# Kernel optimization log

Hardware: AMD Instinct MI355X
Metric: run time of the kernel (lower is better)

Reference implementation:

```python
import jax, jax.numpy as jnp
import numpy as np

NUM_NODES = 50000
NUM_REL_ORIG = 5            # original relation types
NUM_REL = 2 * NUM_REL_ORIG + 1  # augmented: original + inverse + self-loop = 11
F_IN = 128
F_OUT = 128
NUM_EDGES = 800000


def setup_inputs() -> dict:
    key = jax.random.key(0)
    k1, k2, k3, k4, k5, k6 = jax.random.split(key, 6)
    src = jax.random.randint(k1, (NUM_EDGES,), 0, NUM_NODES, dtype=jnp.int32)
    rel = jax.random.randint(k2, (NUM_EDGES,), 0, NUM_REL_ORIG, dtype=jnp.int32)
    dst = jax.random.randint(k3, (NUM_EDGES,), 0, NUM_NODES, dtype=jnp.int32)
    graph = jnp.stack([src, rel, dst], axis=1)  # [E, 3] = (head, relation, tail)
    features = jax.random.normal(k4, (NUM_NODES, F_IN), dtype=jnp.float32)
    # RGCNConv parameters (no basis/block decomposition, bias=False, root_weight=True)
    glorot = lambda k, shape: jax.random.normal(k, shape, dtype=jnp.float32) * jnp.sqrt(2.0 / (shape[-2] + shape[-1]))
    weight = glorot(k5, (NUM_REL, F_IN, F_OUT))  # per-relation weights
    root = glorot(k6, (F_IN, F_OUT))             # root (self) weight
    return {"graph": graph, "features": features, "weight": weight, "root": root}


def reference(graph, features, weight, root):
    N = features.shape[0]
    R = weight.shape[0]
    n_orig = (R - 1) // 2
    src, rel, dst = graph[:, 0], graph[:, 1], graph[:, 2]
    loop = jnp.arange(N, dtype=graph.dtype)
    # augmented edge list: original, inverse, self-loops
    full_src = jnp.concatenate([src, dst, loop])
    full_dst = jnp.concatenate([dst, src, loop])
    full_rel = jnp.concatenate([rel, rel + n_orig, jnp.full((N,), 2 * n_orig, dtype=graph.dtype)])
    # per-(relation, dst-node) mean of source features (PyG RGCNConv aggr='mean'
    # aggregates raw x_j per relation, then applies W_r to the aggregate)
    seg = full_rel * N + full_dst  # [E_full]
    msgs = features[full_src]      # [E_full, F_in] gather
    sums = jax.ops.segment_sum(msgs, seg, num_segments=R * N)           # [R*N, F_in]
    cnts = jax.ops.segment_sum(jnp.ones((seg.shape[0],), features.dtype), seg, num_segments=R * N)
    mean = sums / jnp.maximum(cnts, 1.0)[:, None]
    mean = mean.reshape(R, N, -1)  # [R, N, F_in]
    # out = sum_r mean_r @ W_r + x @ W_root
    out = jnp.einsum('rnf,rfo->no', mean, weight) + features @ root
    return out
```

## Files before the change

### kernel.cpp

```cpp
#include <hip/hip_runtime.h>
#include <hip/hip_bf16.h>

#define NN 50000
#define RO 5
#define RT 11
#define FF 128
#define EE 800000
#define EE2 (2 * EE)
#define NBINS (2 * RO * NN)
#define SLOTS 32
#define DPB 32
#define FEAT_BLKS ((NN * FF / 4) / 256)
#define WT_BLKS ((RT * FF * FF) / 256)

typedef unsigned short u16;
typedef unsigned int u32;
typedef __attribute__((ext_vector_type(4))) unsigned short u16x4;
typedef __attribute__((ext_vector_type(4))) unsigned int u32x4;
typedef __attribute__((ext_vector_type(8))) short bf16x8;
typedef __attribute__((ext_vector_type(4))) float f32x4;

__device__ __forceinline__ u16 f2b(float x) {
  unsigned u = __float_as_uint(x);
  return (u16)((u + 0x7fffu + ((u >> 16) & 1u)) >> 16);
}

__global__ __launch_bounds__(256) void prep_k(const float* __restrict__ f,
                                              const float* __restrict__ w,
                                              const float* __restrict__ root,
                                              u16* __restrict__ fb,
                                              u16* __restrict__ wt) {
  int b = blockIdx.x;
  if (b < FEAT_BLKS) {
    int i = b * 256 + threadIdx.x;
    float4 v = reinterpret_cast<const float4*>(f)[i];
    u16x4 o;
    o.x = f2b(v.x); o.y = f2b(v.y); o.z = f2b(v.z); o.w = f2b(v.w);
    reinterpret_cast<u16x4*>(fb)[i] = o;
  } else if (b < FEAT_BLKS + WT_BLKS) {
    int idx = (b - FEAT_BLKS) * 256 + threadIdx.x;
    int r = idx >> 14;
    int rem = idx & 16383;
    int k = rem >> 7;
    int o = rem & 127;
    float v = w[idx];
    if (r == 10) v += root[rem];
    int chunk = (k >> 3) ^ (o & 7);
    wt[(r << 14) + (o << 7) + (chunk << 3) + (k & 7)] = f2b(v);
  } else {
    if (threadIdx.x < 64) reinterpret_cast<u32*>(fb)[NN * 64 + threadIdx.x] = 0;
  }
}

__global__ __launch_bounds__(256) void fill_k(const int* __restrict__ g,
                                              int* __restrict__ cur,
                                              u16* __restrict__ eidx) {
  const int m = blockIdx.x * 256 + threadIdx.x;
  int e, bin; u16 val;
  if (m < EE) {
    e = m;
    int s = g[3 * e], r = g[3 * e + 1], d = g[3 * e + 2];
    bin = r * NN + d; val = (u16)s;
  } else {
    e = m - EE;
    int d2 = g[3 * e], r = g[3 * e + 1], s2 = g[3 * e + 2];
    bin = (r + RO) * NN + d2; val = (u16)s2;
  }
  int pos = atomicAdd(&cur[bin], 1);
  if (pos < SLOTS) eidx[bin * SLOTS + pos] = val;
}

#define ACCX(p) { a0 += __uint_as_float((p).x << 16); a1 += __uint_as_float((p).x & 0xffff0000u); \
                  a2 += __uint_as_float((p).y << 16); a3 += __uint_as_float((p).y & 0xffff0000u); \
                  a4 += __uint_as_float((p).z << 16); a5 += __uint_as_float((p).z & 0xffff0000u); \
                  a6 += __uint_as_float((p).w << 16); a7 += __uint_as_float((p).w & 0xffff0000u); }
#define ACCY(p) { b0 += __uint_as_float((p).x << 16); b1 += __uint_as_float((p).x & 0xffff0000u); \
                  b2 += __uint_as_float((p).y << 16); b3 += __uint_as_float((p).y & 0xffff0000u); \
                  b4 += __uint_as_float((p).z << 16); b5 += __uint_as_float((p).z & 0xffff0000u); \
                  b6 += __uint_as_float((p).w << 16); b7 += __uint_as_float((p).w & 0xffff0000u); }

__global__ __launch_bounds__(256) void mg_k(const int* __restrict__ cnt,
                                            const u32* __restrict__ eidx32,
                                            const u32x4* __restrict__ fv4,
                                            const u16* __restrict__ fbf,
                                            const u16* __restrict__ wt,
                                            float* __restrict__ out) {
  __shared__ __align__(16) u32x4 Asw[DPB * 16];
  const int tid  = threadIdx.x;
  const int lane = tid & 63;
  const int wv   = tid >> 6;
  const int l15  = lane & 15;
  const int ko   = lane >> 4;
  const int qid  = wv * 4 + ko;
  const int q16  = ko << 4;
  const int base = blockIdx.x * DPB;

  f32x4 acc[2][2];
#pragma unroll
  for (int i = 0; i < 2; ++i)
#pragma unroll
    for (int j = 0; j < 2; ++j) acc[i][j] = (f32x4){0.f, 0.f, 0.f, 0.f};

  const int row0 = qid * 2, row1 = row0 + 1;
  const int d0 = base + row0, d1 = base + row1;
  const bool v0 = d0 < NN, v1 = d1 < NN;

  for (int r = 0; r < 10; ++r) {
    const int seg0 = v0 ? r * NN + d0 : 0;
    const int seg1 = v1 ? r * NN + d1 : 0;
    const int c0 = v0 ? min(cnt[seg0], SLOTS) : 0;
    const int c1 = v1 ? min(cnt[seg1], SLOTS) : 0;
    const u32 sl0 = eidx32[seg0 * 16 + l15];
    const u32 sl1 = eidx32[seg1 * 16 + l15];
    int cmax = max(c0, c1);
    cmax = max(cmax, __shfl_xor(cmax, 16));
    cmax = max(cmax, __shfl_xor(cmax, 32));

    float a0 = 0.f, a1 = 0.f, a2 = 0.f, a3 = 0.f, a4 = 0.f, a5 = 0.f, a6 = 0.f, a7 = 0.f;
    float b0 = 0.f, b1 = 0.f, b2 = 0.f, b3 = 0.f, b4 = 0.f, b5 = 0.f, b6 = 0.f, b7 = 0.f;

    for (int i = 0; i < cmax; i += 4) {
      u32 wa0 = __shfl(sl0, q16 + (i >> 1));
      u32 wa1 = __shfl(sl0, q16 + (i >> 1) + 1);
      u32 wb0 = __shfl(sl1, q16 + (i >> 1));
      u32 wb1 = __shfl(sl1, q16 + (i >> 1) + 1);
      int s0 = (i     < c0) ? (int)(wa0 & 0xffffu) : NN;
      int s1 = (i + 1 < c0) ? (int)(wa0 >> 16)     : NN;
      int s2 = (i + 2 < c0) ? (int)(wa1 & 0xffffu) : NN;
      int s3 = (i + 3 < c0) ? (int)(wa1 >> 16)     : NN;
      int t0 = (i     < c1) ? (int)(wb0 & 0xffffu) : NN;
      int t1 = (i + 1 < c1) ? (int)(wb0 >> 16)     : NN;
      int t2 = (i + 2 < c1) ? (int)(wb1 & 0xffffu) : NN;
      int t3 = (i + 3 < c1) ? (int)(wb1 >> 16)     : NN;
      u32x4 p0 = fv4[s0 * 16 + l15];
      u32x4 p1 = fv4[s1 * 16 + l15];
      u32x4 p2 = fv4[s2 * 16 + l15];
      u32x4 p3 = fv4[s3 * 16 + l15];
      u32x4 p4 = fv4[t0 * 16 + l15];
      u32x4 p5 = fv4[t1 * 16 + l15];
      u32x4 p6 = fv4[t2 * 16 + l15];
      u32x4 p7 = fv4[t3 * 16 + l15];
      ACCX(p0); ACCX(p1); ACCX(p2); ACCX(p3);
      ACCY(p4); ACCY(p5); ACCY(p6); ACCY(p7);
    }

    const float i0 = (c0 > 0) ? 1.0f / (float)c0 : 0.0f;
    const float i1 = (c1 > 0) ? 1.0f / (float)c1 : 0.0f;
    u32x4 m0, m1;
    m0.x = (u32)f2b(a0 * i0) | ((u32)f2b(a1 * i0) << 16);
    m0.y = (u32)f2b(a2 * i0) | ((u32)f2b(a3 * i0) << 16);
    m0.z = (u32)f2b(a4 * i0) | ((u32)f2b(a5 * i0) << 16);
    m0.w = (u32)f2b(a6 * i0) | ((u32)f2b(a7 * i0) << 16);
    m1.x = (u32)f2b(b0 * i1) | ((u32)f2b(b1 * i1) << 16);
    m1.y = (u32)f2b(b2 * i1) | ((u32)f2b(b3 * i1) << 16);
    m1.z = (u32)f2b(b4 * i1) | ((u32)f2b(b5 * i1) << 16);
    m1.w = (u32)f2b(b6 * i1) | ((u32)f2b(b7 * i1) << 16);
    Asw[row0 * 16 + (l15 ^ (row0 & 7))] = m0;
    Asw[row1 * 16 + (l15 ^ (row1 & 7))] = m1;
    __syncthreads();

    const u16* wb = wt + (r << 14);
#pragma unroll
    for (int kc = 0; kc < 4; ++kc) {
      bf16x8 afr[2];
#pragma unroll
      for (int fq = 0; fq < 2; ++fq) {
        const int arow = fq * 16 + l15;
        afr[fq] = *reinterpret_cast<const bf16x8*>(
            &Asw[arow * 16 + ((kc * 4 + ko) ^ (arow & 7))]);
      }
#pragma unroll
      for (int fr = 0; fr < 2; ++fr) {
        const int o = wv * 32 + fr * 16 + l15;
        bf16x8 b = *reinterpret_cast<const bf16x8*>(
            wb + (o << 7) + (((kc * 4 + ko) ^ (o & 7)) << 3));
        acc[0][fr] = __builtin_amdgcn_mfma_f32_16x16x32_bf16(afr[0], b, acc[0][fr], 0, 0, 0);
        acc[1][fr] = __builtin_amdgcn_mfma_f32_16x16x32_bf16(afr[1], b, acc[1][fr], 0, 0, 0);
      }
    }
    __syncthreads();
  }

  {
    const u16* wb = wt + (10 << 14);
#pragma unroll
    for (int kc = 0; kc < 4; ++kc) {
      bf16x8 afr[2];
#pragma unroll
      for (int fq = 0; fq < 2; ++fq) {
        int rowg = base + fq * 16 + l15;
        rowg = (rowg < NN) ? rowg : NN;
        afr[fq] = *reinterpret_cast<const bf16x8*>(
            fbf + (long)rowg * FF + kc * 32 + ko * 8);
      }
#pragma unroll
      for (int fr = 0; fr < 2; ++fr) {
        const int o = wv * 32 + fr * 16 + l15;
        bf16x8 b = *reinterpret_cast<const bf16x8*>(
            wb + (o << 7) + (((kc * 4 + ko) ^ (o & 7)) << 3));
        acc[0][fr] = __builtin_amdgcn_mfma_f32_16x16x32_bf16(afr[0], b, acc[0][fr], 0, 0, 0);
        acc[1][fr] = __builtin_amdgcn_mfma_f32_16x16x32_bf16(afr[1], b, acc[1][fr], 0, 0, 0);
      }
    }
  }

#pragma unroll
  for (int fq = 0; fq < 2; ++fq)
#pragma unroll
    for (int fr = 0; fr < 2; ++fr)
#pragma unroll
      for (int q2 = 0; q2 < 4; ++q2) {
        const int row = base + fq * 16 + ko * 4 + q2;
        if (row < NN) out[row * FF + wv * 32 + fr * 16 + l15] = acc[fq][fr][q2];
      }
}

extern "C" void kernel_launch(void* const* d_in, const int* in_sizes, int n_in,
                              void* d_out, int out_size, void* d_ws, size_t ws_size,
                              hipStream_t stream) {
  const int*   graph  = (const int*)d_in[0];
  const float* feat   = (const float*)d_in[1];
  const float* weight = (const float*)d_in[2];
  const float* root   = (const float*)d_in[3];
  float* out = (float*)d_out;
  char* ws = (char*)d_ws;

  u16* fbf  = (u16*)(ws);
  u16* wt   = (u16*)(ws + 12800512);
  int* cur  = (int*)(ws + 13160960);
  u16* eidx = (u16*)(ws + 15161088);

  hipMemsetAsync(cur, 0, NBINS * sizeof(int), stream);
  prep_k<<<FEAT_BLKS + WT_BLKS + 1, 256, 0, stream>>>(feat, weight, root, fbf, wt);
  fill_k<<<EE2 / 256, 256, 0, stream>>>(graph, cur, eidx);
  mg_k<<<(NN + DPB - 1) / DPB, 256, 0, stream>>>(cur, (const u32*)eidx,
                                                 (const u32x4*)fbf, fbf, wt, out);
}
```

Before: 288.1 us.

## Fuse fill and prep kernels; halve destinations per block in gather-matmul

Merges the edge-bucketing kernel and the feature/weight bf16 conversion kernel into one launch so they can run concurrently. The main kernel now handles 16 destination rows per block instead of 32, so each 16-lane quarter gathers one destination row and the MFMA runs on a single 16-row A tile. The result is twice as many blocks and lower register use, at the cost of reading each weight fragment twice as often overall. Bounds checks are dropped because 50000 divides evenly by 16.

```diff
diff --git a/kernel.cpp b/kernel.cpp
--- a/kernel.cpp
+++ b/kernel.cpp
@@ -9,7 +9,8 @@
 #define EE2 (2 * EE)
 #define NBINS (2 * RO * NN)
 #define SLOTS 32
-#define DPB 32
+#define DPB 16
+#define FILL_BLKS (EE2 / 256)
 #define FEAT_BLKS ((NN * FF / 4) / 256)
 #define WT_BLKS ((RT * FF * FF) / 256)
 
@@ -25,20 +26,37 @@
   return (u16)((u + 0x7fffu + ((u >> 16) & 1u)) >> 16);
 }
 
-__global__ __launch_bounds__(256) void prep_k(const float* __restrict__ f,
-                                              const float* __restrict__ w,
-                                              const float* __restrict__ root,
-                                              u16* __restrict__ fb,
-                                              u16* __restrict__ wt) {
-  int b = blockIdx.x;
-  if (b < FEAT_BLKS) {
-    int i = b * 256 + threadIdx.x;
+__global__ __launch_bounds__(256) void pf_k(const int* __restrict__ g,
+                                            const float* __restrict__ f,
+                                            const float* __restrict__ w,
+                                            const float* __restrict__ root,
+                                            int* __restrict__ cur,
+                                            u16* __restrict__ eidx,
+                                            u16* __restrict__ fb,
+                                            u16* __restrict__ wt) {
+  const int b = blockIdx.x;
+  if (b < FILL_BLKS) {
+    const int m = b * 256 + threadIdx.x;
+    int e, bin; u16 val;
+    if (m < EE) {
+      e = m;
+      int s = g[3 * e], r = g[3 * e + 1], d = g[3 * e + 2];
+      bin = r * NN + d; val = (u16)s;
+    } else {
+      e = m - EE;
+      int d2 = g[3 * e], r = g[3 * e + 1], s2 = g[3 * e + 2];
+      bin = (r + RO) * NN + d2; val = (u16)s2;
+    }
+    int pos = atomicAdd(&cur[bin], 1);
+    if (pos < SLOTS) eidx[bin * SLOTS + pos] = val;
+  } else if (b < FILL_BLKS + FEAT_BLKS) {
+    int i = (b - FILL_BLKS) * 256 + threadIdx.x;
     float4 v = reinterpret_cast<const float4*>(f)[i];
     u16x4 o;
     o.x = f2b(v.x); o.y = f2b(v.y); o.z = f2b(v.z); o.w = f2b(v.w);
     reinterpret_cast<u16x4*>(fb)[i] = o;
-  } else if (b < FEAT_BLKS + WT_BLKS) {
-    int idx = (b - FEAT_BLKS) * 256 + threadIdx.x;
+  } else if (b < FILL_BLKS + FEAT_BLKS + WT_BLKS) {
+    int idx = (b - FILL_BLKS - FEAT_BLKS) * 256 + threadIdx.x;
     int r = idx >> 14;
     int rem = idx & 16383;
     int k = rem >> 7;
@@ -52,32 +70,10 @@
   }
 }
 
-__global__ __launch_bounds__(256) void fill_k(const int* __restrict__ g,
-                                              int* __restrict__ cur,
-                                              u16* __restrict__ eidx) {
-  const int m = blockIdx.x * 256 + threadIdx.x;
-  int e, bin; u16 val;
-  if (m < EE) {
-    e = m;
-    int s = g[3 * e], r = g[3 * e + 1], d = g[3 * e + 2];
-    bin = r * NN + d; val = (u16)s;
-  } else {
-    e = m - EE;
-    int d2 = g[3 * e], r = g[3 * e + 1], s2 = g[3 * e + 2];
-    bin = (r + RO) * NN + d2; val = (u16)s2;
-  }
-  int pos = atomicAdd(&cur[bin], 1);
-  if (pos < SLOTS) eidx[bin * SLOTS + pos] = val;
-}
-
 #define ACCX(p) { a0 += __uint_as_float((p).x << 16); a1 += __uint_as_float((p).x & 0xffff0000u); \
                   a2 += __uint_as_float((p).y << 16); a3 += __uint_as_float((p).y & 0xffff0000u); \
                   a4 += __uint_as_float((p).z << 16); a5 += __uint_as_float((p).z & 0xffff0000u); \
                   a6 += __uint_as_float((p).w << 16); a7 += __uint_as_float((p).w & 0xffff0000u); }
-#define ACCY(p) { b0 += __uint_as_float((p).x << 16); b1 += __uint_as_float((p).x & 0xffff0000u); \
-                  b2 += __uint_as_float((p).y << 16); b3 += __uint_as_float((p).y & 0xffff0000u); \
-                  b4 += __uint_as_float((p).z << 16); b5 += __uint_as_float((p).z & 0xffff0000u); \
-                  b6 += __uint_as_float((p).w << 16); b7 += __uint_as_float((p).w & 0xffff0000u); }
 
 __global__ __launch_bounds__(256) void mg_k(const int* __restrict__ cnt,
                                             const u32* __restrict__ eidx32,
@@ -94,88 +90,55 @@
   const int qid  = wv * 4 + ko;
   const int q16  = ko << 4;
   const int base = blockIdx.x * DPB;
+  const int drow = base + qid;
 
-  f32x4 acc[2][2];
-#pragma unroll
-  for (int i = 0; i < 2; ++i)
-#pragma unroll
-    for (int j = 0; j < 2; ++j) acc[i][j] = (f32x4){0.f, 0.f, 0.f, 0.f};
-
-  const int row0 = qid * 2, row1 = row0 + 1;
-  const int d0 = base + row0, d1 = base + row1;
-  const bool v0 = d0 < NN, v1 = d1 < NN;
+  f32x4 acc[2];
+  acc[0] = (f32x4){0.f, 0.f, 0.f, 0.f};
+  acc[1] = (f32x4){0.f, 0.f, 0.f, 0.f};
 
   for (int r = 0; r < 10; ++r) {
-    const int seg0 = v0 ? r * NN + d0 : 0;
-    const int seg1 = v1 ? r * NN + d1 : 0;
-    const int c0 = v0 ? min(cnt[seg0], SLOTS) : 0;
-    const int c1 = v1 ? min(cnt[seg1], SLOTS) : 0;
-    const u32 sl0 = eidx32[seg0 * 16 + l15];
-    const u32 sl1 = eidx32[seg1 * 16 + l15];
-    int cmax = max(c0, c1);
+    const int seg = r * NN + drow;
+    const int c = min(cnt[seg], SLOTS);
+    const u32 sl = eidx32[seg * 16 + l15];
+    int cmax = c;
     cmax = max(cmax, __shfl_xor(cmax, 16));
     cmax = max(cmax, __shfl_xor(cmax, 32));
 
     float a0 = 0.f, a1 = 0.f, a2 = 0.f, a3 = 0.f, a4 = 0.f, a5 = 0.f, a6 = 0.f, a7 = 0.f;
-    float b0 = 0.f, b1 = 0.f, b2 = 0.f, b3 = 0.f, b4 = 0.f, b5 = 0.f, b6 = 0.f, b7 = 0.f;
-
     for (int i = 0; i < cmax; i += 4) {
-      u32 wa0 = __shfl(sl0, q16 + (i >> 1));
-      u32 wa1 = __shfl(sl0, q16 + (i >> 1) + 1);
-      u32 wb0 = __shfl(sl1, q16 + (i >> 1));
-      u32 wb1 = __shfl(sl1, q16 + (i >> 1) + 1);
-      int s0 = (i     < c0) ? (int)(wa0 & 0xffffu) : NN;
-      int s1 = (i + 1 < c0) ? (int)(wa0 >> 16)     : NN;
-      int s2 = (i + 2 < c0) ? (int)(wa1 & 0xffffu) : NN;
-      int s3 = (i + 3 < c0) ? (int)(wa1 >> 16)     : NN;
-      int t0 = (i     < c1) ? (int)(wb0 & 0xffffu) : NN;
-      int t1 = (i + 1 < c1) ? (int)(wb0 >> 16)     : NN;
-      int t2 = (i + 2 < c1) ? (int)(wb1 & 0xffffu) : NN;
-      int t3 = (i + 3 < c1) ? (int)(wb1 >> 16)     : NN;
+      u32 w0 = __shfl(sl, q16 + (i >> 1));
+      u32 w1 = __shfl(sl, q16 + (i >> 1) + 1);
+      int s0 = (i     < c) ? (int)(w0 & 0xffffu) : NN;
+      int s1 = (i + 1 < c) ? (int)(w0 >> 16)     : NN;
+      int s2 = (i + 2 < c) ? (int)(w1 & 0xffffu) : NN;
+      int s3 = (i + 3 < c) ? (int)(w1 >> 16)     : NN;
       u32x4 p0 = fv4[s0 * 16 + l15];
       u32x4 p1 = fv4[s1 * 16 + l15];
       u32x4 p2 = fv4[s2 * 16 + l15];
       u32x4 p3 = fv4[s3 * 16 + l15];
-      u32x4 p4 = fv4[t0 * 16 + l15];
-      u32x4 p5 = fv4[t1 * 16 + l15];
-      u32x4 p6 = fv4[t2 * 16 + l15];
-      u32x4 p7 = fv4[t3 * 16 + l15];
       ACCX(p0); ACCX(p1); ACCX(p2); ACCX(p3);
-      ACCY(p4); ACCY(p5); ACCY(p6); ACCY(p7);
     }
 
-    const float i0 = (c0 > 0) ? 1.0f / (float)c0 : 0.0f;
-    const float i1 = (c1 > 0) ? 1.0f / (float)c1 : 0.0f;
-    u32x4 m0, m1;
-    m0.x = (u32)f2b(a0 * i0) | ((u32)f2b(a1 * i0) << 16);
-    m0.y = (u32)f2b(a2 * i0) | ((u32)f2b(a3 * i0) << 16);
-    m0.z = (u32)f2b(a4 * i0) | ((u32)f2b(a5 * i0) << 16);
-    m0.w = (u32)f2b(a6 * i0) | ((u32)f2b(a7 * i0) << 16);
-    m1.x = (u32)f2b(b0 * i1) | ((u32)f2b(b1 * i1) << 16);
-    m1.y = (u32)f2b(b2 * i1) | ((u32)f2b(b3 * i1) << 16);
-    m1.z = (u32)f2b(b4 * i1) | ((u32)f2b(b5 * i1) << 16);
-    m1.w = (u32)f2b(b6 * i1) | ((u32)f2b(b7 * i1) << 16);
-    Asw[row0 * 16 + (l15 ^ (row0 & 7))] = m0;
-    Asw[row1 * 16 + (l15 ^ (row1 & 7))] = m1;
+    const float inv = (c > 0) ? 1.0f / (float)c : 0.0f;
+    u32x4 m0;
+    m0.x = (u32)f2b(a0 * inv) | ((u32)f2b(a1 * inv) << 16);
+    m0.y = (u32)f2b(a2 * inv) | ((u32)f2b(a3 * inv) << 16);
+    m0.z = (u32)f2b(a4 * inv) | ((u32)f2b(a5 * inv) << 16);
+    m0.w = (u32)f2b(a6 * inv) | ((u32)f2b(a7 * inv) << 16);
+    Asw[qid * 16 + (l15 ^ (qid & 7))] = m0;
     __syncthreads();
 
     const u16* wb = wt + (r << 14);
 #pragma unroll
     for (int kc = 0; kc < 4; ++kc) {
-      bf16x8 afr[2];
-#pragma unroll
-      for (int fq = 0; fq < 2; ++fq) {
-        const int arow = fq * 16 + l15;
-        afr[fq] = *reinterpret_cast<const bf16x8*>(
-            &Asw[arow * 16 + ((kc * 4 + ko) ^ (arow & 7))]);
-      }
+      bf16x8 a = *reinterpret_cast<const bf16x8*>(
+          &Asw[l15 * 16 + ((kc * 4 + ko) ^ (l15 & 7))]);
 #pragma unroll
       for (int fr = 0; fr < 2; ++fr) {
         const int o = wv * 32 + fr * 16 + l15;
-        bf16x8 b = *reinterpret_cast<const bf16x8*>(
+        bf16x8 bfrag = *reinterpret_cast<const bf16x8*>(
             wb + (o << 7) + (((kc * 4 + ko) ^ (o & 7)) << 3));
-        acc[0][fr] = __builtin_amdgcn_mfma_f32_16x16x32_bf16(afr[0], b, acc[0][fr], 0, 0, 0);
-        acc[1][fr] = __builtin_amdgcn_mfma_f32_16x16x32_bf16(afr[1], b, acc[1][fr], 0, 0, 0);
+        acc[fr] = __builtin_amdgcn_mfma_f32_16x16x32_bf16(a, bfrag, acc[fr], 0, 0, 0);
       }
     }
     __syncthreads();
@@ -185,34 +148,23 @@
     const u16* wb = wt + (10 << 14);
 #pragma unroll
     for (int kc = 0; kc < 4; ++kc) {
-      bf16x8 afr[2];
-#pragma unroll
-      for (int fq = 0; fq < 2; ++fq) {
-        int rowg = base + fq * 16 + l15;
-        rowg = (rowg < NN) ? rowg : NN;
-        afr[fq] = *reinterpret_cast<const bf16x8*>(
-            fbf + (long)rowg * FF + kc * 32 + ko * 8);
-      }
+      bf16x8 a = *reinterpret_cast<const bf16x8*>(
+          fbf + (long)(base + l15) * FF + kc * 32 + ko * 8);
 #pragma unroll
       for (int fr = 0; fr < 2; ++fr) {
         const int o = wv * 32 + fr * 16 + l15;
-        bf16x8 b = *reinterpret_cast<const bf16x8*>(
+        bf16x8 bfrag = *reinterpret_cast<const bf16x8*>(
             wb + (o << 7) + (((kc * 4 + ko) ^ (o & 7)) << 3));
-        acc[0][fr] = __builtin_amdgcn_mfma_f32_16x16x32_bf16(afr[0], b, acc[0][fr], 0, 0, 0);
-        acc[1][fr] = __builtin_amdgcn_mfma_f32_16x16x32_bf16(afr[1], b, acc[1][fr], 0, 0, 0);
+        acc[fr] = __builtin_amdgcn_mfma_f32_16x16x32_bf16(a, bfrag, acc[fr], 0, 0, 0);
       }
     }
   }
 
 #pragma unroll
-  for (int fq = 0; fq < 2; ++fq)
+  for (int fr = 0; fr < 2; ++fr)
 #pragma unroll
-    for (int fr = 0; fr < 2; ++fr)
-#pragma unroll
-      for (int q2 = 0; q2 < 4; ++q2) {
-        const int row = base + fq * 16 + ko * 4 + q2;
-        if (row < NN) out[row * FF + wv * 32 + fr * 16 + l15] = acc[fq][fr][q2];
-      }
+    for (int q2 = 0; q2 < 4; ++q2)
+      out[(base + ko * 4 + q2) * FF + wv * 32 + fr * 16 + l15] = acc[fr][q2];
 }
 
 extern "C" void kernel_launch(void* const* d_in, const int* in_sizes, int n_in,
@@ -231,8 +183,8 @@
   u16* eidx = (u16*)(ws + 15161088);
 
   hipMemsetAsync(cur, 0, NBINS * sizeof(int), stream);
-  prep_k<<<FEAT_BLKS + WT_BLKS + 1, 256, 0, stream>>>(feat, weight, root, fbf, wt);
-  fill_k<<<EE2 / 256, 256, 0, stream>>>(graph, cur, eidx);
-  mg_k<<<(NN + DPB - 1) / DPB, 256, 0, stream>>>(cur, (const u32*)eidx,
-                                                 (const u32x4*)fbf, fbf, wt, out);
+  pf_k<<<FILL_BLKS + FEAT_BLKS + WT_BLKS + 1, 256, 0, stream>>>(
+      graph, feat, weight, root, cur, eidx, fbf, wt);
+  mg_k<<<NN / DPB, 256, 0, stream>>>(cur, (const u32*)eidx,
+                                     (const u32x4*)fbf, fbf, wt, out);
 }
```

Result: slower. 305.6 us (+6.1%).
